# Kernel optimization log

Measured on AMD Instinct MI355X. Metric: run time of the kernel, lower is better.

Reference implementation:

```python
import jax, jax.numpy as jnp
import numpy as np

N, E = 100000, 3200000          # nodes, edges (avg degree 32)
F_IN, HID, OUT2, NUM_CLASSES = 128, 64, 2, 4


def setup_inputs() -> dict:
    key = jax.random.key(0)
    ks = jax.random.split(key, 8)
    x = jax.random.normal(ks[0], (N, F_IN), dtype=jnp.float32)
    edge_index = jax.random.randint(ks[1], (2, E), 0, N, dtype=jnp.int32)
    # Glorot-ish inits for the linear weights, zero biases (PyG GCNConv default)
    W1 = jax.random.normal(ks[2], (F_IN, HID), dtype=jnp.float32) / np.float32(np.sqrt(F_IN))
    b1 = jnp.zeros((HID,), jnp.float32)
    W2 = jax.random.normal(ks[3], (HID, OUT2), dtype=jnp.float32) / np.float32(np.sqrt(HID))
    b2 = jnp.zeros((OUT2,), jnp.float32)
    Wc = jax.random.normal(ks[4], (OUT2, NUM_CLASSES), dtype=jnp.float32) / np.float32(np.sqrt(OUT2))
    bc = jnp.zeros((NUM_CLASSES,), jnp.float32)
    return {"x": x, "edge_index": edge_index, "W1": W1, "b1": b1,
            "W2": W2, "b2": b2, "Wc": Wc, "bc": bc}


def gcn_conv(x, W, b, src, dst):
    """PyG GCNConv: out = D^-1/2 (A+I) D^-1/2 (x W) + b, sum aggregation."""
    n = x.shape[0]
    # degree of A+I: 1 (self loop) + in-degree at target nodes
    deg = jnp.ones((n,), x.dtype).at[dst].add(jnp.asarray(1.0, x.dtype))
    dinv = jax.lax.rsqrt(deg)                      # deg >= 1 always
    xw = x @ W                                      # [n, out] dense GEMM first
    norm = dinv[src] * dinv[dst]                    # [E]
    agg = jax.ops.segment_sum(xw[src] * norm[:, None], dst, num_segments=n)
    agg = agg + xw * (dinv * dinv)[:, None]         # self-loop contribution
    return agg + b


def reference(x, edge_index, W1, b1, W2, b2, Wc, bc):
    src, dst = edge_index[0], edge_index[1]
    h = jnp.tanh(gcn_conv(x, W1, b1, src, dst))
    h = jnp.tanh(gcn_conv(h, W2, b2, src, dst))
    out = h @ Wc + bc
    return (out, h)
```

## Files before the change

kernel.cpp:

```cpp
#include <hip/hip_runtime.h>
#include <hip/hip_bf16.h>
#include <hip/hip_fp16.h>


#define NB2 261
#define CAP2 9472
#define MAXB 400
#define BIN_CHUNK 4096

__global__ __launch_bounds__(256) void k_bin(const int* __restrict__ src,
                                             const int* __restrict__ dst,
                                             int E, int nbuckets,
                                             int* __restrict__ binCnt,
                                             int* __restrict__ bins) {
    __shared__ int stageP[BIN_CHUNK];
    __shared__ unsigned short stageB[BIN_CHUNK];
    __shared__ int lcnt[MAXB];
    __shared__ int lbase[MAXB + 1];
    __shared__ int gbase[MAXB];
    __shared__ int lpos[MAXB];
    int base = blockIdx.x * BIN_CHUNK;
    if (base >= E) return;
    int cnt_here = min(BIN_CHUNK, E - base);

    for (int b = threadIdx.x; b < nbuckets; b += 256) lcnt[b] = 0;
    __syncthreads();
    int p_[16], b_[16];
    #pragma unroll
    for (int k = 0; k < 16; k++) {
        int i = base + threadIdx.x + k * 256;
        if (i < E) {
            int s = __builtin_nontemporal_load(src + i);
            int d = __builtin_nontemporal_load(dst + i);
            int b = d / NB2;
            b_[k] = b;
            p_[k] = s | ((d - b * NB2) << 17);
            atomicAdd(&lcnt[b], 1);
        } else {
            b_[k] = -1;
        }
    }
    __syncthreads();
    if (threadIdx.x == 0) {
        int run = 0;
        for (int b = 0; b < nbuckets; b++) { lbase[b] = run; run += lcnt[b]; }
        lbase[nbuckets] = run;
    }
    __syncthreads();
    for (int b = threadIdx.x; b < nbuckets; b += 256) {
        gbase[b] = atomicAdd(&binCnt[b], lcnt[b]);
        lpos[b] = lbase[b];
    }
    __syncthreads();
    #pragma unroll
    for (int k = 0; k < 16; k++) {
        if (b_[k] >= 0) {
            int pos = atomicAdd(&lpos[b_[k]], 1);
            stageP[pos] = p_[k];
            stageB[pos] = (unsigned short)b_[k];
        }
    }
    __syncthreads();
    for (int i = threadIdx.x; i < cnt_here; i += 256) {
        int b = stageB[i];
        int gi = gbase[b] + (i - lbase[b]);
        if (gi < CAP2) bins[(size_t)b * CAP2 + gi] = stageP[i];
    }
}

__global__ void k_bscan(const int* __restrict__ binCnt, int* __restrict__ bbase,
                        int nbuckets, int* __restrict__ rowptr, int N) {
    if (blockIdx.x == 0 && threadIdx.x == 0) {
        int run = 0;
        for (int b = 0; b < nbuckets; b++) {
            bbase[b] = run;
            run += min(binCnt[b], CAP2);
        }
        bbase[nbuckets] = run;
        rowptr[N] = run;
    }
}

__global__ __launch_bounds__(256) void k_csr(const int* __restrict__ bins,
                                             const int* __restrict__ binCnt,
                                             const int* __restrict__ bbase,
                                             int* __restrict__ rowptr,
                                             int* __restrict__ csr_src,
                                             float* __restrict__ dinv, int N) {
    __shared__ int hist[NB2 + 1];
    __shared__ int lrp[NB2 + 1];
    __shared__ int lcur[NB2];
    __shared__ int stage[CAP2];
    int b = blockIdx.x;
    int lo = b * NB2;
    int nn = min(NB2, N - lo);
    if (nn <= 0) return;
    int m = min(binCnt[b], CAP2);
    const int* bp = bins + (size_t)b * CAP2;

    for (int t = threadIdx.x; t < nn; t += 256) hist[t] = 0;
    __syncthreads();
    for (int i = threadIdx.x; i < m; i += 256) {
        unsigned int e = (unsigned int)__builtin_nontemporal_load(bp + i);
        atomicAdd(&hist[e >> 17], 1);
    }
    __syncthreads();
    if (threadIdx.x == 0) {
        int run = 0;
        for (int t = 0; t < nn; t++) { lrp[t] = run; run += hist[t]; }
        lrp[nn] = run;
    }
    __syncthreads();
    int gb = bbase[b];
    for (int t = threadIdx.x; t < nn; t += 256) {
        rowptr[lo + t] = gb + lrp[t];
        lcur[t] = lrp[t];
        dinv[lo + t] = rsqrtf(1.0f + (float)hist[t]);
    }
    __syncthreads();
    for (int i = threadIdx.x; i < m; i += 256) {
        unsigned int e = (unsigned int)__builtin_nontemporal_load(bp + i);
        int p = atomicAdd(&lcur[e >> 17], 1);
        stage[p] = (int)(e & 0x1FFFF);
    }
    __syncthreads();
    for (int i = threadIdx.x; i < m; i += 256) {
        csr_src[gb + i] = stage[i];
    }
}

__global__ __launch_bounds__(256) void k_gemm1(const float* __restrict__ x,
                                               const float* __restrict__ W1,
                                               const float* __restrict__ dinv,
                                               __half* __restrict__ xw, int n) {
    int lrow = threadIdx.x & 63;
    int c0 = __builtin_amdgcn_readfirstlane((threadIdx.x >> 6) * 16);
    int row = blockIdx.x * 64 + lrow;
    if (row > n) return;
    if (row == n) {
        float4 z = make_float4(0.f, 0.f, 0.f, 0.f);
        float4* op = reinterpret_cast<float4*>(xw + (size_t)row * 64 + c0);
        op[0] = z;
        op[1] = z;
        return;
    }
    const float* xr = x + (size_t)row * 128;

    float acc[16];
    #pragma unroll
    for (int c = 0; c < 16; ++c) acc[c] = 0.f;

    for (int k4 = 0; k4 < 32; ++k4) {
        float4 xv = *reinterpret_cast<const float4*>(xr + k4 * 4);
        const float* wp = W1 + (size_t)k4 * 4 * 64 + c0;
        #pragma unroll
        for (int c = 0; c < 16; ++c) {
            acc[c] = fmaf(xv.x, wp[c], acc[c]);
            acc[c] = fmaf(xv.y, wp[64 + c], acc[c]);
            acc[c] = fmaf(xv.z, wp[128 + c], acc[c]);
            acc[c] = fmaf(xv.w, wp[192 + c], acc[c]);
        }
    }

    float di = dinv[row];
    __half2 hb[8];
    #pragma unroll
    for (int c = 0; c < 8; ++c)
        hb[c] = __floats2half2_rn(acc[2 * c] * di, acc[2 * c + 1] * di);
    float4* op = reinterpret_cast<float4*>(xw + (size_t)row * 64 + c0);
    const float4* hp = reinterpret_cast<const float4*>(hb);
    op[0] = hp[0];
    op[1] = hp[1];
}

__global__ void k_agg1(const int* __restrict__ rowptr, const int* __restrict__ csr_src,
                       const float* __restrict__ dinv, const __half* __restrict__ xw1s,
                       const float* __restrict__ b1, const float* __restrict__ W2,
                       float* __restrict__ xw2s, int n) {
    int lane = threadIdx.x & 63;
    int q    = lane >> 4;
    int ln   = lane & 15;
    float4 b1v = *reinterpret_cast<const float4*>(b1 + 4 * ln);
    float4 w2a = *reinterpret_cast<const float4*>(W2 + 8 * ln);
    float4 w2b = *reinterpret_cast<const float4*>(W2 + 8 * ln + 4);
    const float2* xp2 = reinterpret_cast<const float2*>(xw1s);

    int wid  = blockIdx.x * (blockDim.x >> 6) + (threadIdx.x >> 6);
    int wtot = gridDim.x * (blockDim.x >> 6);
    int nquad = (n + 3) >> 2;
    for (int qd = wid; qd < nquad; qd += wtot) {
        int d = 4 * qd + q;
        bool ok = d < n;
        int base = 0, cnt = 0;
        float dd = 0.f;
        if (ok) { base = rowptr[d]; cnt = rowptr[d + 1] - base; dd = dinv[d]; }
        float a0 = 0.f, a1 = 0.f, a2 = 0.f, a3 = 0.f;

        int nch = (cnt + 15) >> 4;
        int ncm = max(nch, __shfl_xor(nch, 16));
        ncm = max(ncm, __shfl_xor(ncm, 32));

        for (int c = 0; c < ncm; ++c) {
            int rel = c * 16 + ln;
            int v = (rel < cnt) ? __builtin_nontemporal_load(csr_src + base + rel) : n;
            float2 r[16];
            #pragma unroll
            for (int k = 0; k < 16; ++k) {
                int sv = __shfl(v, (q << 4) | k);
                r[k] = xp2[(size_t)sv * 16 + ln];
            }
            #pragma unroll
            for (int k = 0; k < 16; ++k) {
                float2 f01 = __half22float2(__builtin_bit_cast(__half2, r[k].x));
                float2 f23 = __half22float2(__builtin_bit_cast(__half2, r[k].y));
                a0 += f01.x;
                a1 += f01.y;
                a2 += f23.x;
                a3 += f23.y;
            }
        }

        float p0 = 0.f, p1 = 0.f;
        if (ok) {
            float2 r = xp2[(size_t)d * 16 + ln];
            float2 s01 = __half22float2(__builtin_bit_cast(__half2, r.x));
            float2 s23 = __half22float2(__builtin_bit_cast(__half2, r.y));
            float h0 = tanhf((a0 + s01.x) * dd + b1v.x);
            float h1 = tanhf((a1 + s01.y) * dd + b1v.y);
            float h2 = tanhf((a2 + s23.x) * dd + b1v.z);
            float h3 = tanhf((a3 + s23.y) * dd + b1v.w);
            p0 = h0 * w2a.x + h1 * w2a.z + h2 * w2b.x + h3 * w2b.z;
            p1 = h0 * w2a.y + h1 * w2a.w + h2 * w2b.y + h3 * w2b.w;
        }
        #pragma unroll
        for (int m = 8; m >= 1; m >>= 1) {
            p0 += __shfl_xor(p0, m);
            p1 += __shfl_xor(p1, m);
        }
        if (ok && ln == 0)
            *reinterpret_cast<float2*>(xw2s + (size_t)d * 2) = make_float2(p0 * dd, p1 * dd);
    }
}

__global__ void k_agg2(const int* __restrict__ rowptr, const int* __restrict__ csr_src,
                       const float* __restrict__ dinv, const float* __restrict__ xw2s,
                       const float* __restrict__ b2, const float* __restrict__ Wc,
                       const float* __restrict__ bc,
                       float* __restrict__ out, float* __restrict__ hout, int n) {
    int lane = threadIdx.x & 63;
    int slot = lane >> 1;
    int f = lane & 1;
    float b2v = b2[f];
    int wid = blockIdx.x * (blockDim.x >> 6) + (threadIdx.x >> 6);
    int wtot = gridDim.x * (blockDim.x >> 6);
    for (int d = wid; d < n; d += wtot) {
        int base = rowptr[d], end = rowptr[d + 1];
        float dd = dinv[d];
        float acc = (slot == 0) ? xw2s[(size_t)d * 2 + f] : 0.f;
        for (int j = base + slot; j < end; j += 32) {
            int s = __builtin_nontemporal_load(csr_src + j);
            acc += xw2s[(size_t)s * 2 + f];
        }
        #pragma unroll
        for (int m = 32; m >= 2; m >>= 1) acc += __shfl_xor(acc, m);
        float h = tanhf(acc * dd + b2v);
        float other = __shfl_xor(h, 1);
        if (lane == 0) {
            *reinterpret_cast<float2*>(hout + (size_t)d * 2) = make_float2(h, other);
            float4 o;
            o.x = fmaf(h, Wc[0], fmaf(other, Wc[4], bc[0]));
            o.y = fmaf(h, Wc[1], fmaf(other, Wc[5], bc[1]));
            o.z = fmaf(h, Wc[2], fmaf(other, Wc[6], bc[2]));
            o.w = fmaf(h, Wc[3], fmaf(other, Wc[7], bc[3]));
            *reinterpret_cast<float4*>(out + (size_t)d * 4) = o;
        }
    }
}

extern "C" void kernel_launch(void* const* d_in, const int* in_sizes, int n_in,
                              void* d_out, int out_size, void* d_ws, size_t ws_size,
                              hipStream_t stream) {
    const float* x  = (const float*)d_in[0];
    const int* ei   = (const int*)d_in[1];
    const float* W1 = (const float*)d_in[2];
    const float* b1 = (const float*)d_in[3];
    const float* W2 = (const float*)d_in[4];
    const float* b2 = (const float*)d_in[5];
    const float* Wc = (const float*)d_in[6];
    const float* bc = (const float*)d_in[7];

    const int N = in_sizes[0] / 128;
    const int E = in_sizes[1] / 2;
    const int* src = ei;
    const int* dst = ei + E;

    float* out  = (float*)d_out;
    float* hout = out + (size_t)N * 4;

    const int NBK = (N + NB2 - 1) / NB2;

    char* ws = (char*)d_ws;
    int*    csr_src = (int*)ws;
    char*   uni     = (char*)(csr_src + E);
    int*    bins    = (int*)uni;
    __half* xw1s    = (__half*)uni;
    size_t uni_sz   = (size_t)NBK * CAP2 * sizeof(int);
    size_t xw1_sz   = (size_t)(N + 1) * 64 * sizeof(__half);
    char*  after    = uni + (uni_sz > xw1_sz ? uni_sz : xw1_sz);
    int*   binCnt   = (int*)after;
    int*   bbase    = binCnt + NBK;
    float* dinv     = (float*)(bbase + NBK + 1);
    float* xw2s     = dinv + N;
    int*   rowptr   = (int*)(xw2s + (size_t)N * 2);

    (void)hipMemsetAsync(binCnt, 0, (size_t)NBK * sizeof(int), stream);
    k_bin<<<(E + BIN_CHUNK - 1) / BIN_CHUNK, 256, 0, stream>>>(src, dst, E, NBK, binCnt, bins);
    k_bscan<<<1, 64, 0, stream>>>(binCnt, bbase, NBK, rowptr, N);
    k_csr<<<NBK, 256, 0, stream>>>(bins, binCnt, bbase, rowptr, csr_src, dinv, N);

    k_gemm1<<<(N + 64) / 64, 256, 0, stream>>>(x, W1, dinv, xw1s, N);
    k_agg1<<<2048, 256, 0, stream>>>(rowptr, csr_src, dinv, xw1s, b1, W2, xw2s, N);
    k_agg2<<<2048, 256, 0, stream>>>(rowptr, csr_src, dinv, xw2s, b2, Wc, bc, out, hout, N);
}
```

Baseline: 216.1 us.

## Process eight nodes per wavefront in layer-1 aggregation with packed half2 accumulation

```diff
diff --git a/kernel.cpp b/kernel.cpp
--- a/kernel.cpp
+++ b/kernel.cpp
@@ -178,62 +178,76 @@
                        const float* __restrict__ b1, const float* __restrict__ W2,
                        float* __restrict__ xw2s, int n) {
     int lane = threadIdx.x & 63;
-    int q    = lane >> 4;
-    int ln   = lane & 15;
-    float4 b1v = *reinterpret_cast<const float4*>(b1 + 4 * ln);
-    float4 w2a = *reinterpret_cast<const float4*>(W2 + 8 * ln);
-    float4 w2b = *reinterpret_cast<const float4*>(W2 + 8 * ln + 4);
-    const float2* xp2 = reinterpret_cast<const float2*>(xw1s);
+    int oc   = lane >> 3;
+    int ln   = lane & 7;
+    float4 b1a = *reinterpret_cast<const float4*>(b1 + 8 * ln);
+    float4 b1b = *reinterpret_cast<const float4*>(b1 + 8 * ln + 4);
+    float4 w2q[4];
+    #pragma unroll
+    for (int i = 0; i < 4; ++i)
+        w2q[i] = *reinterpret_cast<const float4*>(W2 + 16 * ln + 4 * i);
+    const float4* xp4 = reinterpret_cast<const float4*>(xw1s);
 
     int wid  = blockIdx.x * (blockDim.x >> 6) + (threadIdx.x >> 6);
     int wtot = gridDim.x * (blockDim.x >> 6);
-    int nquad = (n + 3) >> 2;
-    for (int qd = wid; qd < nquad; qd += wtot) {
-        int d = 4 * qd + q;
+    int noct = (n + 7) >> 3;
+    for (int od = wid; od < noct; od += wtot) {
+        int d = 8 * od + oc;
         bool ok = d < n;
         int base = 0, cnt = 0;
         float dd = 0.f;
         if (ok) { base = rowptr[d]; cnt = rowptr[d + 1] - base; dd = dinv[d]; }
-        float a0 = 0.f, a1 = 0.f, a2 = 0.f, a3 = 0.f;
-
-        int nch = (cnt + 15) >> 4;
-        int ncm = max(nch, __shfl_xor(nch, 16));
-        ncm = max(ncm, __shfl_xor(ncm, 32));
-
-        for (int c = 0; c < ncm; ++c) {
-            int rel = c * 16 + ln;
+        float af[8];
+        #pragma unroll
+        for (int i = 0; i < 8; ++i) af[i] = 0.f;
+
+        int nch = (cnt + 7) >> 3;
+        nch = max(nch, __shfl_xor(nch, 8));
+        nch = max(nch, __shfl_xor(nch, 16));
+        nch = max(nch, __shfl_xor(nch, 32));
+
+        for (int c = 0; c < nch; ++c) {
+            int rel = c * 8 + ln;
             int v = (rel < cnt) ? __builtin_nontemporal_load(csr_src + base + rel) : n;
-            float2 r[16];
+            __half2 h0 = __half2(0.f, 0.f), h1 = __half2(0.f, 0.f);
+            __half2 h2 = __half2(0.f, 0.f), h3 = __half2(0.f, 0.f);
             #pragma unroll
-            for (int k = 0; k < 16; ++k) {
-                int sv = __shfl(v, (q << 4) | k);
-                r[k] = xp2[(size_t)sv * 16 + ln];
+            for (int k = 0; k < 8; ++k) {
+                int sv = __shfl(v, (oc << 3) | k);
+                float4 r = xp4[(size_t)sv * 8 + ln];
+                h0 = __hadd2(h0, __builtin_bit_cast(__half2, r.x));
+                h1 = __hadd2(h1, __builtin_bit_cast(__half2, r.y));
+                h2 = __hadd2(h2, __builtin_bit_cast(__half2, r.z));
+                h3 = __hadd2(h3, __builtin_bit_cast(__half2, r.w));
             }
-            #pragma unroll
-            for (int k = 0; k < 16; ++k) {
-                float2 f01 = __half22float2(__builtin_bit_cast(__half2, r[k].x));
-                float2 f23 = __half22float2(__builtin_bit_cast(__half2, r[k].y));
-                a0 += f01.x;
-                a1 += f01.y;
-                a2 += f23.x;
-                a3 += f23.y;
-            }
+            float2 f0 = __half22float2(h0), f1 = __half22float2(h1);
+            float2 f2 = __half22float2(h2), f3 = __half22float2(h3);
+            af[0] += f0.x; af[1] += f0.y; af[2] += f1.x; af[3] += f1.y;
+            af[4] += f2.x; af[5] += f2.y; af[6] += f3.x; af[7] += f3.y;
         }
 
         float p0 = 0.f, p1 = 0.f;
         if (ok) {
-            float2 r = xp2[(size_t)d * 16 + ln];
-            float2 s01 = __half22float2(__builtin_bit_cast(__half2, r.x));
-            float2 s23 = __half22float2(__builtin_bit_cast(__half2, r.y));
-            float h0 = tanhf((a0 + s01.x) * dd + b1v.x);
-            float h1 = tanhf((a1 + s01.y) * dd + b1v.y);
-            float h2 = tanhf((a2 + s23.x) * dd + b1v.z);
-            float h3 = tanhf((a3 + s23.y) * dd + b1v.w);
-            p0 = h0 * w2a.x + h1 * w2a.z + h2 * w2b.x + h3 * w2b.z;
-            p1 = h0 * w2a.y + h1 * w2a.w + h2 * w2b.y + h3 * w2b.w;
+            float4 rs = xp4[(size_t)d * 8 + ln];
+            float2 s0 = __half22float2(__builtin_bit_cast(__half2, rs.x));
+            float2 s1 = __half22float2(__builtin_bit_cast(__half2, rs.y));
+            float2 s2 = __half22float2(__builtin_bit_cast(__half2, rs.z));
+            float2 s3 = __half22float2(__builtin_bit_cast(__half2, rs.w));
+            float sf[8] = {s0.x, s0.y, s1.x, s1.y, s2.x, s2.y, s3.x, s3.y};
+            float bf[8] = {b1a.x, b1a.y, b1a.z, b1a.w, b1b.x, b1b.y, b1b.z, b1b.w};
+            #pragma unroll
+            for (int i = 0; i < 8; ++i) {
+                float h = tanhf((af[i] + sf[i]) * dd + bf[i]);
+                float wA = (i & 1) ? ((i & 2) ? ((i < 4) ? w2q[1].z : w2q[3].z) : ((i < 4) ? w2q[0].z : w2q[2].z))
+                                   : ((i & 2) ? ((i < 4) ? w2q[1].x : w2q[3].x) : ((i < 4) ? w2q[0].x : w2q[2].x));
+                float wB = (i & 1) ? ((i & 2) ? ((i < 4) ? w2q[1].w : w2q[3].w) : ((i < 4) ? w2q[0].w : w2q[2].w))
+                                   : ((i & 2) ? ((i < 4) ? w2q[1].y : w2q[3].y) : ((i < 4) ? w2q[0].y : w2q[2].y));
+                p0 = fmaf(h, wA, p0);
+                p1 = fmaf(h, wB, p1);
+            }
         }
         #pragma unroll
-        for (int m = 8; m >= 1; m >>= 1) {
+        for (int m = 4; m >= 1; m >>= 1) {
             p0 += __shfl_xor(p0, m);
             p1 += __shfl_xor(p1, m);
         }
```

Result: slower. 222.2 us (+2.8%).

## Slice xw1 into feature-sliced planes and split layer-1 aggregation across feature teams

Applied to the files above, without the earlier changes.

```diff
diff --git a/kernel.cpp b/kernel.cpp
--- a/kernel.cpp
+++ b/kernel.cpp
@@ -137,11 +137,12 @@
     int c0 = __builtin_amdgcn_readfirstlane((threadIdx.x >> 6) * 16);
     int row = blockIdx.x * 64 + lrow;
     if (row > n) return;
+    float4* xp = reinterpret_cast<float4*>(xw);
+    int sl0 = c0 >> 3;
     if (row == n) {
         float4 z = make_float4(0.f, 0.f, 0.f, 0.f);
-        float4* op = reinterpret_cast<float4*>(xw + (size_t)row * 64 + c0);
-        op[0] = z;
-        op[1] = z;
+        xp[(size_t)sl0 * (n + 1) + row] = z;
+        xp[(size_t)(sl0 + 1) * (n + 1) + row] = z;
         return;
     }
     const float* xr = x + (size_t)row * 128;
@@ -167,78 +168,86 @@
     #pragma unroll
     for (int c = 0; c < 8; ++c)
         hb[c] = __floats2half2_rn(acc[2 * c] * di, acc[2 * c + 1] * di);
-    float4* op = reinterpret_cast<float4*>(xw + (size_t)row * 64 + c0);
     const float4* hp = reinterpret_cast<const float4*>(hb);
-    op[0] = hp[0];
-    op[1] = hp[1];
+    xp[(size_t)sl0 * (n + 1) + row] = hp[0];
+    xp[(size_t)(sl0 + 1) * (n + 1) + row] = hp[1];
 }
 
 __global__ void k_agg1(const int* __restrict__ rowptr, const int* __restrict__ csr_src,
                        const float* __restrict__ dinv, const __half* __restrict__ xw1s,
                        const float* __restrict__ b1, const float* __restrict__ W2,
                        float* __restrict__ xw2s, int n) {
+    int team = blockIdx.x & 7;
     int lane = threadIdx.x & 63;
-    int q    = lane >> 4;
-    int ln   = lane & 15;
-    float4 b1v = *reinterpret_cast<const float4*>(b1 + 4 * ln);
-    float4 w2a = *reinterpret_cast<const float4*>(W2 + 8 * ln);
-    float4 w2b = *reinterpret_cast<const float4*>(W2 + 8 * ln + 4);
-    const float2* xp2 = reinterpret_cast<const float2*>(xw1s);
-
-    int wid  = blockIdx.x * (blockDim.x >> 6) + (threadIdx.x >> 6);
-    int wtot = gridDim.x * (blockDim.x >> 6);
-    int nquad = (n + 3) >> 2;
-    for (int qd = wid; qd < nquad; qd += wtot) {
-        int d = 4 * qd + q;
+    int half = lane >> 5;
+    int L = lane & 31;
+    int f = L & 7;
+    float b1v = b1[8 * team + f];
+    float w20 = W2[(8 * team + f) * 2 + 0];
+    float w21 = W2[(8 * team + f) * 2 + 1];
+    const float4* sl = reinterpret_cast<const float4*>(xw1s) + (size_t)team * (n + 1);
+
+    int wid  = (blockIdx.x >> 3) * (blockDim.x >> 6) + (threadIdx.x >> 6);
+    int wtot = (gridDim.x >> 3) * (blockDim.x >> 6);
+    int npair = (n + 1) >> 1;
+    for (int pr = wid; pr < npair; pr += wtot) {
+        int d = 2 * pr + half;
         bool ok = d < n;
         int base = 0, cnt = 0;
         float dd = 0.f;
         if (ok) { base = rowptr[d]; cnt = rowptr[d + 1] - base; dd = dinv[d]; }
-        float a0 = 0.f, a1 = 0.f, a2 = 0.f, a3 = 0.f;
-
-        int nch = (cnt + 15) >> 4;
-        int ncm = max(nch, __shfl_xor(nch, 16));
-        ncm = max(ncm, __shfl_xor(ncm, 32));
-
-        for (int c = 0; c < ncm; ++c) {
-            int rel = c * 16 + ln;
-            int v = (rel < cnt) ? __builtin_nontemporal_load(csr_src + base + rel) : n;
-            float2 r[16];
-            #pragma unroll
-            for (int k = 0; k < 16; ++k) {
-                int sv = __shfl(v, (q << 4) | k);
-                r[k] = xp2[(size_t)sv * 16 + ln];
-            }
-            #pragma unroll
-            for (int k = 0; k < 16; ++k) {
-                float2 f01 = __half22float2(__builtin_bit_cast(__half2, r[k].x));
-                float2 f23 = __half22float2(__builtin_bit_cast(__half2, r[k].y));
-                a0 += f01.x;
-                a1 += f01.y;
-                a2 += f23.x;
-                a3 += f23.y;
-            }
-        }
-
-        float p0 = 0.f, p1 = 0.f;
-        if (ok) {
-            float2 r = xp2[(size_t)d * 16 + ln];
-            float2 s01 = __half22float2(__builtin_bit_cast(__half2, r.x));
-            float2 s23 = __half22float2(__builtin_bit_cast(__half2, r.y));
-            float h0 = tanhf((a0 + s01.x) * dd + b1v.x);
-            float h1 = tanhf((a1 + s01.y) * dd + b1v.y);
-            float h2 = tanhf((a2 + s23.x) * dd + b1v.z);
-            float h3 = tanhf((a3 + s23.y) * dd + b1v.w);
-            p0 = h0 * w2a.x + h1 * w2a.z + h2 * w2b.x + h3 * w2b.z;
-            p1 = h0 * w2a.y + h1 * w2a.w + h2 * w2b.y + h3 * w2b.w;
-        }
+
+        int s0i = (ok && L == 0) ? d : n;
+        float4 rs = sl[s0i];
+        __half2 a0 = __builtin_bit_cast(__half2, rs.x);
+        __half2 a1 = __builtin_bit_cast(__half2, rs.y);
+        __half2 a2 = __builtin_bit_cast(__half2, rs.z);
+        __half2 a3 = __builtin_bit_cast(__half2, rs.w);
+
+        int nch = (cnt + 31) >> 5;
+        for (int c = 0; c < nch; ++c) {
+            int rel = c * 32 + L;
+            int s = (rel < cnt) ? __builtin_nontemporal_load(csr_src + base + rel) : n;
+            float4 r = sl[s];
+            a0 = __hadd2(a0, __builtin_bit_cast(__half2, r.x));
+            a1 = __hadd2(a1, __builtin_bit_cast(__half2, r.y));
+            a2 = __hadd2(a2, __builtin_bit_cast(__half2, r.z));
+            a3 = __hadd2(a3, __builtin_bit_cast(__half2, r.w));
+        }
+
+        float2 f0 = __half22float2(a0), f1 = __half22float2(a1);
+        float2 f2 = __half22float2(a2), f3 = __half22float2(a3);
+        float af0 = f0.x, af1 = f0.y, af2 = f1.x, af3 = f1.y;
+        float af4 = f2.x, af5 = f2.y, af6 = f3.x, af7 = f3.y;
         #pragma unroll
-        for (int m = 8; m >= 1; m >>= 1) {
-            p0 += __shfl_xor(p0, m);
-            p1 += __shfl_xor(p1, m);
-        }
-        if (ok && ln == 0)
-            *reinterpret_cast<float2*>(xw2s + (size_t)d * 2) = make_float2(p0 * dd, p1 * dd);
+        for (int m = 16; m >= 1; m >>= 1) {
+            af0 += __shfl_xor(af0, m);
+            af1 += __shfl_xor(af1, m);
+            af2 += __shfl_xor(af2, m);
+            af3 += __shfl_xor(af3, m);
+            af4 += __shfl_xor(af4, m);
+            af5 += __shfl_xor(af5, m);
+            af6 += __shfl_xor(af6, m);
+            af7 += __shfl_xor(af7, m);
+        }
+        float lo01 = (f & 1) ? af1 : af0;
+        float lo23 = (f & 1) ? af3 : af2;
+        float lo45 = (f & 1) ? af5 : af4;
+        float lo67 = (f & 1) ? af7 : af6;
+        float q0 = (f & 2) ? lo23 : lo01;
+        float q1 = (f & 2) ? lo67 : lo45;
+        float av = (f & 4) ? q1 : q0;
+
+        float h = ok ? tanhf(av * dd + b1v) : 0.f;
+        float p0 = h * w20;
+        float p1 = h * w21;
+        p0 += __shfl_xor(p0, 1);  p1 += __shfl_xor(p1, 1);
+        p0 += __shfl_xor(p0, 2);  p1 += __shfl_xor(p1, 2);
+        p0 += __shfl_xor(p0, 4);  p1 += __shfl_xor(p1, 4);
+        if (ok && L == 0) {
+            atomicAdd(&xw2s[(size_t)d * 2 + 0], p0 * dd);
+            atomicAdd(&xw2s[(size_t)d * 2 + 1], p1 * dd);
+        }
     }
 }
 
@@ -319,6 +328,7 @@
     k_csr<<<NBK, 256, 0, stream>>>(bins, binCnt, bbase, rowptr, csr_src, dinv, N);
 
     k_gemm1<<<(N + 64) / 64, 256, 0, stream>>>(x, W1, dinv, xw1s, N);
+    (void)hipMemsetAsync(xw2s, 0, (size_t)N * 2 * sizeof(float), stream);
     k_agg1<<<2048, 256, 0, stream>>>(rowptr, csr_src, dinv, xw1s, b1, W2, xw2s, N);
     k_agg2<<<2048, 256, 0, stream>>>(rowptr, csr_src, dinv, xw2s, b2, Wc, bc, out, hout, N);
 }
```

Result: slower. 390.7 us (+80.8%).
